# Optimization experiments

Hardware: AMD Instinct MI355X
Metric: run time of the kernel (lower is better)

Reference implementation:

```python
import jax, jax.numpy as jnp
import numpy as np

BATCH = 4
N_MELS, T_LEN, PATCH = 128, 512, 16
D_MODEL, D_INNER, D_STATE, DT_RANK, D_CONV = 512, 1024, 16, 32, 4
DEPTH, N_CLASSES = 4, 10


def _silu(x):
    return x * jax.nn.sigmoid(x)


def _ln(x, w, b):
    m = x.mean(-1, keepdims=True)
    v = ((x - m) ** 2).mean(-1, keepdims=True)
    return (x - m) * jax.lax.rsqrt(v + 1e-5) * w + b


def _causal_conv(x, w, b):
    # x: (B, L, D); w: (D, K) depthwise causal conv (mamba conv1d)
    K, L = w.shape[-1], x.shape[1]
    xp = jnp.pad(x, ((0, 0), (K - 1, 0), (0, 0)))
    y = sum(xp[:, k:k + L, :] * w[:, k] for k in range(K))
    return y + b


def _ssm(xc, conv_w, conv_b, xproj_w, dtproj_w, dtproj_b, A_log, Dp):
    # One directional selective scan (mamba S6).
    u = _silu(_causal_conv(xc, conv_w, conv_b))              # (B,L,Di)
    xdbl = jnp.einsum('bld,ed->ble', u, xproj_w)             # (B,L,dt_rank+2S)
    dtr, Bm, Cm = jnp.split(xdbl, [DT_RANK, DT_RANK + D_STATE], axis=-1)
    dt = jax.nn.softplus(jnp.einsum('blr,dr->bld', dtr, dtproj_w) + dtproj_b)
    A = -jnp.exp(A_log)                                      # (Di,S)
    dA = jnp.exp(dt[..., None] * A)                          # (B,L,Di,S)
    dBu = (dt * u)[..., None] * Bm[:, :, None, :]            # (B,L,Di,S)

    def comb(e1, e2):
        a1, b1 = e1
        a2, b2 = e2
        return a1 * a2, a2 * b1 + b2

    _, h = jax.lax.associative_scan(comb, (dA, dBu), axis=1)  # parallel linear recurrence
    return jnp.einsum('blds,bls->bld', h, Cm) + u * Dp


def _forward(x, patch_w, patch_b, in_proj_w, conv_w_f, conv_b_f, conv_w_b, conv_b_b,
             xproj_w_f, xproj_w_b, dtproj_w_f, dtproj_b_f, dtproj_w_b, dtproj_b_b,
             A_log_f, A_log_b, D_f, D_b, out_proj_w, norm_w, norm_b,
             normf_w, normf_b, ln_w, ln_b, fc1_w, fc1_b, fc2_w, fc2_b):
    B = x.shape[0]
    # Patch embed: conv with kernel == stride -> reshape + einsum
    xp = x.reshape(B, 1, N_MELS // PATCH, PATCH, T_LEN // PATCH, PATCH)
    tok = jnp.einsum('bchpwq,dcpq->bhwd', xp, patch_w) + patch_b
    h = tok.reshape(B, -1, D_MODEL)                           # (B, 256, D)
    for i in range(DEPTH):
        xn = _ln(h, norm_w[i], norm_b[i])
        xz = jnp.einsum('bld,ed->ble', xn, in_proj_w[i])
        xc, z = jnp.split(xz, 2, axis=-1)
        y_f = _ssm(xc, conv_w_f[i], conv_b_f[i], xproj_w_f[i],
                   dtproj_w_f[i], dtproj_b_f[i], A_log_f[i], D_f[i])
        y_b = jnp.flip(_ssm(jnp.flip(xc, 1), conv_w_b[i], conv_b_b[i], xproj_w_b[i],
                            dtproj_w_b[i], dtproj_b_b[i], A_log_b[i], D_b[i]), 1)
        y = (y_f + y_b) * _silu(z)                            # bimamba v2: fwd + flipped bwd, gated
        h = h + jnp.einsum('bld,ed->ble', y, out_proj_w[i])
    h = _ln(h, normf_w, normf_b)
    feat = h.mean(axis=1)                                     # pooled features (B, D)
    c = _ln(feat, ln_w, ln_b)
    c = jnp.maximum(c @ fc1_w.T + fc1_b, 0.0)
    return c @ fc2_w.T + fc2_b


def setup_inputs() -> dict:
    ks = iter(jax.random.split(jax.random.key(0), 64))

    def rn(shape, s=0.02):
        return jax.random.normal(next(ks), shape, jnp.float32) * s

    inp = {}
    inp['x'] = jax.random.normal(next(ks), (BATCH, 1, N_MELS, T_LEN), jnp.float32)
    inp['patch_w'] = rn((D_MODEL, 1, PATCH, PATCH))
    inp['patch_b'] = jnp.zeros((D_MODEL,), jnp.float32)
    inp['in_proj_w'] = rn((DEPTH, 2 * D_INNER, D_MODEL))
    A_init = jnp.log(jnp.tile(jnp.arange(1, D_STATE + 1, dtype=jnp.float32), (DEPTH, D_INNER, 1)))
    for sfx in ('f', 'b'):
        inp[f'conv_w_{sfx}'] = rn((DEPTH, D_INNER, D_CONV), 0.2)
        inp[f'conv_b_{sfx}'] = jnp.zeros((DEPTH, D_INNER), jnp.float32)
        inp[f'xproj_w_{sfx}'] = rn((DEPTH, DT_RANK + 2 * D_STATE, D_INNER))
        inp[f'dtproj_w_{sfx}'] = rn((DEPTH, D_INNER, DT_RANK), 0.1)
        inp[f'dtproj_b_{sfx}'] = jnp.full((DEPTH, D_INNER), -4.6, jnp.float32)  # softplus -> dt ~ 0.01
        inp[f'A_log_{sfx}'] = A_init
        inp[f'D_{sfx}'] = jnp.ones((DEPTH, D_INNER), jnp.float32)
    inp['out_proj_w'] = rn((DEPTH, D_MODEL, D_INNER))
    inp['norm_w'] = jnp.ones((DEPTH, D_MODEL), jnp.float32)
    inp['norm_b'] = jnp.zeros((DEPTH, D_MODEL), jnp.float32)
    inp['normf_w'] = jnp.ones((D_MODEL,), jnp.float32)
    inp['normf_b'] = jnp.zeros((D_MODEL,), jnp.float32)
    inp['ln_w'] = jnp.ones((D_MODEL,), jnp.float32)
    inp['ln_b'] = jnp.zeros((D_MODEL,), jnp.float32)
    inp['fc1_w'] = rn((512, D_MODEL))
    inp['fc1_b'] = jnp.zeros((512,), jnp.float32)
    inp['fc2_w'] = rn((N_CLASSES, 512))
    inp['fc2_b'] = jnp.zeros((N_CLASSES,), jnp.float32)
    return inp


def reference(x, patch_w, patch_b, in_proj_w, conv_w_f, conv_b_f, conv_w_b, conv_b_b,
              xproj_w_f, xproj_w_b, dtproj_w_f, dtproj_b_f, dtproj_w_b, dtproj_b_b,
              A_log_f, A_log_b, D_f, D_b, out_proj_w, norm_w, norm_b,
              normf_w, normf_b, ln_w, ln_b, fc1_w, fc1_b, fc2_w, fc2_b):
    return _forward(x, patch_w, patch_b, in_proj_w, conv_w_f, conv_b_f, conv_w_b, conv_b_b,
                    xproj_w_f, xproj_w_b, dtproj_w_f, dtproj_b_f, dtproj_w_b, dtproj_b_b,
                    A_log_f, A_log_b, D_f, D_b, out_proj_w, norm_w, norm_b,
                    normf_w, normf_b, ln_w, ln_b, fc1_w, fc1_b, fc2_w, fc2_b)
```

## Files before the change

kernel.cpp:

```cpp
#include <hip/hip_runtime.h>


#define BB 4
#define LL 256
#define DM 512
#define DI 1024
#define LDST 40

typedef unsigned short u16;
typedef unsigned int u32;
typedef __attribute__((ext_vector_type(8))) short s8v;
typedef __attribute__((ext_vector_type(4))) float f4v;

__device__ __forceinline__ float silu_f(float x){ return x/(1.f+__expf(-x)); }
__device__ __forceinline__ float b2f(u16 u){
  union { u32 i; float f; } v; v.i = ((u32)u) << 16; return v.f;
}
__device__ __forceinline__ void b2x2(u32 w, float& lo, float& hi){
  union { u32 i; float f; } a, b;
  a.i = w << 16; b.i = w & 0xffff0000u;
  lo = a.f; hi = b.f;
}
__device__ __forceinline__ u16 f2bf(float f){
  union { float f; u32 u; } v; v.f = f;
  u32 r = (v.u + 0x7fffu + ((v.u >> 16) & 1u)) >> 16;
  return (u16)r;
}

__device__ __forceinline__ float row_sum16(float p){
  union { float f; int i; } v, r;
  v.f = p;
  r.i = __builtin_amdgcn_update_dpp(0, v.i, 0x111, 0xF, 0xF, true); v.f += r.f;
  r.i = __builtin_amdgcn_update_dpp(0, v.i, 0x112, 0xF, 0xF, true); v.f += r.f;
  r.i = __builtin_amdgcn_update_dpp(0, v.i, 0x114, 0xF, 0xF, true); v.f += r.f;
  r.i = __builtin_amdgcn_update_dpp(0, v.i, 0x118, 0xF, 0xF, true); v.f += r.f;
  return v.f;
}

__device__ __forceinline__ void block_reduce2(float& a, float& b, float* sc, int nw){
  int lane = threadIdx.x & 63, wid = threadIdx.x >> 6;
#pragma unroll
  for (int o = 32; o > 0; o >>= 1){
    a += __shfl_down(a, o, 64);
    b += __shfl_down(b, o, 64);
  }
  if (lane == 0){ sc[wid*2] = a; sc[wid*2+1] = b; }
  __syncthreads();
  float ta = 0.f, tb = 0.f;
  for (int i = 0; i < nw; ++i){ ta += sc[i*2]; tb += sc[i*2+1]; }
  a = ta; b = tb;
}

__global__ __launch_bounds__(256) void convert_w(const float* __restrict__ inW,
    const float* __restrict__ outW, const float* __restrict__ xwF,
    const float* __restrict__ xwB, const float* __restrict__ dtwF,
    const float* __restrict__ dtwB, u16* __restrict__ inHi, u16* __restrict__ inLo,
    u16* __restrict__ outHi, u16* __restrict__ outLo, u16* __restrict__ xwHi,
    u16* __restrict__ xwLo, u16* __restrict__ dtwHi, u16* __restrict__ dtwLo){
  int idx = blockIdx.x*256 + threadIdx.x;
  const float4* src; ushort4* dh; ushort4* dl;
  if (idx < 262144){
    src = (const float4*)inW + idx;
    dh = (ushort4*)inHi + idx; dl = (ushort4*)inLo + idx;
  } else if (idx < 393216){
    int j = idx - 262144;
    src = (const float4*)outW + j;
    dh = (ushort4*)outHi + j; dl = (ushort4*)outLo + j;
  } else if (idx < 409600){
    int j = idx - 393216;
    src = (const float4*)xwF + j;
    dh = (ushort4*)xwHi + j; dl = (ushort4*)xwLo + j;
  } else if (idx < 425984){
    int j = idx - 409600;
    src = (const float4*)xwB + j;
    dh = (ushort4*)(xwHi + 65536) + j; dl = (ushort4*)(xwLo + 65536) + j;
  } else if (idx < 434176){
    int j = idx - 425984;
    src = (const float4*)dtwF + j;
    dh = (ushort4*)dtwHi + j; dl = (ushort4*)dtwLo + j;
  } else {
    int j = idx - 434176;
    src = (const float4*)dtwB + j;
    dh = (ushort4*)(dtwHi + 32768) + j; dl = (ushort4*)(dtwLo + 32768) + j;
  }
  float4 v = *src;
  ushort4 h, l;
  h.x = f2bf(v.x); l.x = f2bf(v.x - b2f(h.x));
  h.y = f2bf(v.y); l.y = f2bf(v.y - b2f(h.y));
  h.z = f2bf(v.z); l.z = f2bf(v.z - b2f(h.z));
  h.w = f2bf(v.w); l.w = f2bf(v.w - b2f(h.w));
  *dh = h; *dl = l;
}

__global__ __launch_bounds__(256) void patch_embed(const float* __restrict__ x,
    const float* __restrict__ pw, const float* __restrict__ pb, float* __restrict__ h){
  __shared__ float xs[8*256];
  int blk = blockIdx.x;
  int b = blk >> 6, ph = (blk >> 3) & 7, pg = (blk >> 1) & 3, dh = blk & 1;
  int t = threadIdx.x;
  for (int idx = t; idx < 2048; idx += 256){
    int j = idx >> 8, pix = idx & 255, p = pix >> 4, q = pix & 15;
    xs[idx] = x[(size_t)(b*128 + ph*16 + p)*512 + pg*128 + j*16 + q];
  }
  __syncthreads();
  int d = dh*256 + t;
  float acc[8] = {};
  const float* wr = pw + (size_t)d*256;
  for (int i = 0; i < 256; i += 8){
    float4 w0 = *(const float4*)(wr + i);
    float4 w1 = *(const float4*)(wr + i + 4);
    float wf[8] = {w0.x,w0.y,w0.z,w0.w,w1.x,w1.y,w1.z,w1.w};
#pragma unroll
    for (int j = 0; j < 8; ++j){
#pragma unroll
      for (int jj = 0; jj < 8; ++jj)
        acc[j] = fmaf(xs[j*256 + i + jj], wf[jj], acc[j]);
    }
  }
  float bias = pb[d];
#pragma unroll
  for (int j = 0; j < 8; ++j)
    h[(size_t)(b*256 + ph*32 + pg*8 + j)*512 + d] = acc[j] + bias;
}

__global__ __launch_bounds__(256) void prep_ln(const float* __restrict__ x,
    const float* __restrict__ w, const float* __restrict__ bias, int wOff,
    u16* __restrict__ hiO, u16* __restrict__ loO){
  __shared__ float sc[8];
  int row = blockIdx.x, t = threadIdx.x;
  const float* xr = x + (size_t)row*DM;
  float v0 = xr[t], v1 = xr[t + 256];
  float s = v0 + v1, ss = v0*v0 + v1*v1;
  block_reduce2(s, ss, sc, 4);
  float mean = s * (1.f/512.f);
  float var = ss * (1.f/512.f) - mean*mean;
  float inv = rsqrtf(var + 1e-5f);
  float o0 = (v0 - mean)*inv*w[wOff + t]       + bias[wOff + t];
  float o1 = (v1 - mean)*inv*w[wOff + t + 256] + bias[wOff + t + 256];
  u16 h0 = f2bf(o0), h1 = f2bf(o1);
  hiO[(size_t)row*DM + t]       = h0;
  hiO[(size_t)row*DM + t + 256] = h1;
  loO[(size_t)row*DM + t]       = f2bf(o0 - b2f(h0));
  loO[(size_t)row*DM + t + 256] = f2bf(o1 - b2f(h1));
}

__global__ __launch_bounds__(256) void prep_gate(const float* __restrict__ ybuf,
    const float* __restrict__ xz, u16* __restrict__ gHi, u16* __restrict__ gLo){
  int row = blockIdx.x, t = threadIdx.x;
  int c = t*4;
  float4 yf = *(const float4*)(ybuf + (size_t)row*DI + c);
  float4 yb = *(const float4*)(ybuf + 1048576 + (size_t)row*DI + c);
  float4 zv = *(const float4*)(xz + (size_t)row*2048 + 1024 + c);
  float g0 = (yf.x + yb.x)*silu_f(zv.x);
  float g1 = (yf.y + yb.y)*silu_f(zv.y);
  float g2 = (yf.z + yb.z)*silu_f(zv.z);
  float g3 = (yf.w + yb.w)*silu_f(zv.w);
  ushort4 h, l;
  h.x = f2bf(g0); l.x = f2bf(g0 - b2f(h.x));
  h.y = f2bf(g1); l.y = f2bf(g1 - b2f(h.y));
  h.z = f2bf(g2); l.z = f2bf(g2 - b2f(h.z));
  h.w = f2bf(g3); l.w = f2bf(g3 - b2f(h.w));
  *(ushort4*)(gHi + (size_t)row*DI + c) = h;
  *(ushort4*)(gLo + (size_t)row*DI + c) = l;
}

__global__ __launch_bounds__(256) void gemm_bf16(const u16* __restrict__ Ahi_g,
    const u16* __restrict__ Alo_g, int As, const u16* __restrict__ Bhi_g,
    const u16* __restrict__ Blo_g, int Bs, float* __restrict__ C, int Cs,
    int K, int addFlag){
  __shared__ __align__(16) u16 Ah[64*LDST], Al[64*LDST], Bh[64*LDST], Bl[64*LDST];
  int bm = blockIdx.y*64, bn = blockIdx.x*64;
  int t = threadIdx.x;
  int sr = t >> 2, sc8 = (t & 3)*8;
  int lane = t & 63, wv = t >> 6, ml = lane & 15, quad = lane >> 4;
  int mq = wv >> 1, nq = wv & 1;
  f4v acc[2][2] = {};
  for (int k0 = 0; k0 < K; k0 += 32){
    *(uint4*)&Ah[sr*LDST + sc8] = *(const uint4*)(Ahi_g + (size_t)(bm + sr)*As + k0 + sc8);
    *(uint4*)&Al[sr*LDST + sc8] = *(const uint4*)(Alo_g + (size_t)(bm + sr)*As + k0 + sc8);
    *(uint4*)&Bh[sr*LDST + sc8] = *(const uint4*)(Bhi_g + (size_t)(bn + sr)*Bs + k0 + sc8);
    *(uint4*)&Bl[sr*LDST + sc8] = *(const uint4*)(Blo_g + (size_t)(bn + sr)*Bs + k0 + sc8);
    __syncthreads();
    s8v ah[2], al2[2], bh2[2], bl2[2];
#pragma unroll
    for (int mt = 0; mt < 2; ++mt){
      int row = mq*32 + mt*16 + ml;
      ah[mt]  = *(s8v*)&Ah[row*LDST + quad*8];
      al2[mt] = *(s8v*)&Al[row*LDST + quad*8];
    }
#pragma unroll
    for (int nt = 0; nt < 2; ++nt){
      int col = nq*32 + nt*16 + ml;
      bh2[nt] = *(s8v*)&Bh[col*LDST + quad*8];
      bl2[nt] = *(s8v*)&Bl[col*LDST + quad*8];
    }
#pragma unroll
    for (int mt = 0; mt < 2; ++mt)
#pragma unroll
      for (int nt = 0; nt < 2; ++nt){
        acc[mt][nt] = __builtin_amdgcn_mfma_f32_16x16x32_bf16(ah[mt],  bh2[nt], acc[mt][nt], 0, 0, 0);
        acc[mt][nt] = __builtin_amdgcn_mfma_f32_16x16x32_bf16(al2[mt], bh2[nt], acc[mt][nt], 0, 0, 0);
        acc[mt][nt] = __builtin_amdgcn_mfma_f32_16x16x32_bf16(ah[mt],  bl2[nt], acc[mt][nt], 0, 0, 0);
      }
    __syncthreads();
  }
#pragma unroll
  for (int mt = 0; mt < 2; ++mt)
#pragma unroll
    for (int nt = 0; nt < 2; ++nt)
#pragma unroll
      for (int r = 0; r < 4; ++r){
        float* cp = C + (size_t)(bm + mq*32 + mt*16 + quad*4 + r)*Cs +
                    bn + nq*32 + nt*16 + ml;
        if (addFlag) *cp += acc[mt][nt][r];
        else         *cp  = acc[mt][nt][r];
      }
}

__global__ __launch_bounds__(256) void conv_silu_split(const float* __restrict__ xz,
    const float* __restrict__ cwF, const float* __restrict__ cbF,
    const float* __restrict__ cwB, const float* __restrict__ cbB,
    int cwOff, int cbOff, u16* __restrict__ uHi, u16* __restrict__ uLo){
  int blk = blockIdx.x;
  int dir = blk >> 8, rem = blk & 255, b = rem >> 6, lg = rem & 63;
  int l0 = lg*4;
  const float* cw = dir ? cwB : cwF;
  const float* cb = dir ? cbB : cbF;
  int t = threadIdx.x;
  int rbase = (dir*BB + b)*LL;
  for (int dd = 0; dd < 4; ++dd){
    int d = t + dd*256;
    float4 w4 = *(const float4*)(cw + cwOff + d*4);
    float wf[4] = {w4.x, w4.y, w4.z, w4.w};
    float bias = cb[cbOff + d];
#pragma unroll
    for (int r = 0; r < 4; ++r){
      int l = l0 + r;
      float acc = bias;
#pragma unroll
      for (int k = 0; k < 4; ++k){
        int li = l + k - 3;
        if (li >= 0){
          int sl = dir ? (LL-1-li) : li;
          acc = fmaf(xz[(size_t)(b*LL + sl)*2048 + d], wf[k], acc);
        }
      }
      float uval = silu_f(acc);
      u16 h = f2bf(uval);
      uHi[(size_t)(rbase + l)*DI + d] = h;
      uLo[(size_t)(rbase + l)*DI + d] = f2bf(uval - b2f(h));
    }
  }
}

__global__ __launch_bounds__(256) void gemm_xproj(const u16* __restrict__ uHi,
    const u16* __restrict__ uLo, const u16* __restrict__ xwHi,
    const u16* __restrict__ xwLo, float* __restrict__ xdbl,
    u16* __restrict__ dtrHi, u16* __restrict__ dtrLo){
  __shared__ __align__(16) u16 Ah[64*LDST], Al[64*LDST], Bh[64*LDST], Bl[64*LDST];
  int bm = blockIdx.y*64;
  int dir = bm >> 10;
  const u16* BhG = xwHi + dir*65536;
  const u16* BlG = xwLo + dir*65536;
  int t = threadIdx.x;
  int sr = t >> 2, sc8 = (t & 3)*8;
  int lane = t & 63, wv = t >> 6, ml = lane & 15, quad = lane >> 4;
  int mq = wv >> 1, nq = wv & 1;
  f4v acc[2][2] = {};
  for (int k0 = 0; k0 < 1024; k0 += 32){
    *(uint4*)&Ah[sr*LDST + sc8] = *(const uint4*)(uHi + (size_t)(bm + sr)*1024 + k0 + sc8);
    *(uint4*)&Al[sr*LDST + sc8] = *(const uint4*)(uLo + (size_t)(bm + sr)*1024 + k0 + sc8);
    *(uint4*)&Bh[sr*LDST + sc8] = *(const uint4*)(BhG + (size_t)sr*1024 + k0 + sc8);
    *(uint4*)&Bl[sr*LDST + sc8] = *(const uint4*)(BlG + (size_t)sr*1024 + k0 + sc8);
    __syncthreads();
    s8v ah[2], al2[2], bh2[2], bl2[2];
#pragma unroll
    for (int mt = 0; mt < 2; ++mt){
      int row = mq*32 + mt*16 + ml;
      ah[mt]  = *(s8v*)&Ah[row*LDST + quad*8];
      al2[mt] = *(s8v*)&Al[row*LDST + quad*8];
    }
#pragma unroll
    for (int nt = 0; nt < 2; ++nt){
      int col = nq*32 + nt*16 + ml;
      bh2[nt] = *(s8v*)&Bh[col*LDST + quad*8];
      bl2[nt] = *(s8v*)&Bl[col*LDST + quad*8];
    }
#pragma unroll
    for (int mt = 0; mt < 2; ++mt)
#pragma unroll
      for (int nt = 0; nt < 2; ++nt){
        acc[mt][nt] = __builtin_amdgcn_mfma_f32_16x16x32_bf16(ah[mt],  bh2[nt], acc[mt][nt], 0, 0, 0);
        acc[mt][nt] = __builtin_amdgcn_mfma_f32_16x16x32_bf16(al2[mt], bh2[nt], acc[mt][nt], 0, 0, 0);
        acc[mt][nt] = __builtin_amdgcn_mfma_f32_16x16x32_bf16(ah[mt],  bl2[nt], acc[mt][nt], 0, 0, 0);
      }
    __syncthreads();
  }
#pragma unroll
  for (int mt = 0; mt < 2; ++mt)
#pragma unroll
    for (int nt = 0; nt < 2; ++nt){
      int col = nq*32 + nt*16 + ml;
#pragma unroll
      for (int r = 0; r < 4; ++r){
        int row = bm + mq*32 + mt*16 + quad*4 + r;
        float v = acc[mt][nt][r];
        xdbl[(size_t)row*64 + col] = v;
        if (nq == 0){
          u16 h = f2bf(v);
          dtrHi[(size_t)row*32 + col] = h;
          dtrLo[(size_t)row*32 + col] = f2bf(v - b2f(h));
        }
      }
    }
}

__global__ __launch_bounds__(256) void gemm_dt(const u16* __restrict__ dtrHi,
    const u16* __restrict__ dtrLo, const u16* __restrict__ dtwHi,
    const u16* __restrict__ dtwLo, const float* __restrict__ dtbF,
    const float* __restrict__ dtbB, int bOff, float* __restrict__ dtOut){
  __shared__ __align__(16) u16 Ah[64*LDST], Al[64*LDST], Bh[64*LDST], Bl[64*LDST];
  int bm = blockIdx.y*64, bn = blockIdx.x*64;
  int dir = bm >> 10;
  const u16* BhG = dtwHi + dir*32768;
  const u16* BlG = dtwLo + dir*32768;
  const float* dtb = dir ? dtbB : dtbF;
  int t = threadIdx.x;
  int sr = t >> 2, sc8 = (t & 3)*8;
  int lane = t & 63, wv = t >> 6, ml = lane & 15, quad = lane >> 4;
  int mq = wv >> 1, nq = wv & 1;
  *(uint4*)&Ah[sr*LDST + sc8] = *(const uint4*)(dtrHi + (size_t)(bm + sr)*32 + sc8);
  *(uint4*)&Al[sr*LDST + sc8] = *(const uint4*)(dtrLo + (size_t)(bm + sr)*32 + sc8);
  *(uint4*)&Bh[sr*LDST + sc8] = *(const uint4*)(BhG + (size_t)(bn + sr)*32 + sc8);
  *(uint4*)&Bl[sr*LDST + sc8] = *(const uint4*)(BlG + (size_t)(bn + sr)*32 + sc8);
  __syncthreads();
  f4v acc[2][2] = {};
  s8v ah[2], al2[2], bh2[2], bl2[2];
#pragma unroll
  for (int mt = 0; mt < 2; ++mt){
    int row = mq*32 + mt*16 + ml;
    ah[mt]  = *(s8v*)&Ah[row*LDST + quad*8];
    al2[mt] = *(s8v*)&Al[row*LDST + quad*8];
  }
#pragma unroll
  for (int nt = 0; nt < 2; ++nt){
    int col = nq*32 + nt*16 + ml;
    bh2[nt] = *(s8v*)&Bh[col*LDST + quad*8];
    bl2[nt] = *(s8v*)&Bl[col*LDST + quad*8];
  }
#pragma unroll
  for (int mt = 0; mt < 2; ++mt)
#pragma unroll
    for (int nt = 0; nt < 2; ++nt){
      acc[mt][nt] = __builtin_amdgcn_mfma_f32_16x16x32_bf16(ah[mt],  bh2[nt], acc[mt][nt], 0, 0, 0);
      acc[mt][nt] = __builtin_amdgcn_mfma_f32_16x16x32_bf16(al2[mt], bh2[nt], acc[mt][nt], 0, 0, 0);
      acc[mt][nt] = __builtin_amdgcn_mfma_f32_16x16x32_bf16(ah[mt],  bl2[nt], acc[mt][nt], 0, 0, 0);
    }
#pragma unroll
  for (int mt = 0; mt < 2; ++mt)
#pragma unroll
    for (int nt = 0; nt < 2; ++nt){
      int col = bn + nq*32 + nt*16 + ml;
      float bias = dtb[bOff + col];
#pragma unroll
      for (int r = 0; r < 4; ++r){
        int row = bm + mq*32 + mt*16 + quad*4 + r;
        float sv = acc[mt][nt][r] + bias;
        dtOut[(size_t)row*1024 + col] = (sv > 15.f) ? sv : log1pf(__expf(sv));
      }
    }
}

__global__ __launch_bounds__(256) void scan_coal(const float* __restrict__ dt,
    const u16* __restrict__ uHi, const u16* __restrict__ uLo,
    const float* __restrict__ xd,
    const float* __restrict__ AlogF, const float* __restrict__ AlogB,
    const float* __restrict__ DF, const float* __restrict__ DB,
    int aOff, int dOff, float* __restrict__ y){
  __shared__ __align__(16) float dtuT[16][516];
  __shared__ __align__(16) float BCT[16][516];
  __shared__ __align__(16) float ytile[128][16];
  int blk = blockIdx.x;
  int dir = blk >> 8, b = (blk >> 6) & 3, dg = blk & 63;
  int t = threadIdx.x;
  int rbase = (dir*BB + b)*LL;
  const float* Alog = dir ? AlogB : AlogF;
  const float* Dpt  = dir ? DB : DF;
  {
    int q = t & 3, lb = t >> 2;
    for (int pass = 0; pass < 4; ++pass){
      int l = pass*64 + lb;
      size_t base = (size_t)(rbase + l)*DI + dg*16 + q*4;
      float4 dv = *(const float4*)(dt + base);
      uint2 uh = *(const uint2*)(uHi + base);
      uint2 ul = *(const uint2*)(uLo + base);
      float h0,h1,h2,h3,l0f,l1f,l2f,l3f;
      b2x2(uh.x, h0, h1); b2x2(uh.y, h2, h3);
      b2x2(ul.x, l0f, l1f); b2x2(ul.y, l2f, l3f);
      float2 p0 = {dv.x, h0 + l0f}, p1 = {dv.y, h1 + l1f};
      float2 p2 = {dv.z, h2 + l2f}, p3 = {dv.w, h3 + l3f};
      *(float2*)&dtuT[q*4+0][l*2] = p0;
      *(float2*)&dtuT[q*4+1][l*2] = p1;
      *(float2*)&dtuT[q*4+2][l*2] = p2;
      *(float2*)&dtuT[q*4+3][l*2] = p3;
    }
  }
  {
    int h8 = t & 7, lb = t >> 3;
    for (int pass = 0; pass < 8; ++pass){
      int l = pass*32 + lb;
      float4 v = *(const float4*)(xd + (size_t)(rbase + l)*64 + 32 + h8*4);
      if (h8 < 4){
        int s0 = h8*4;
        BCT[s0+0][l*2] = v.x; BCT[s0+1][l*2] = v.y;
        BCT[s0+2][l*2] = v.z; BCT[s0+3][l*2] = v.w;
      } else {
        int s0 = (h8-4)*4;
        BCT[s0+0][l*2+1] = v.x; BCT[s0+1][l*2+1] = v.y;
        BCT[s0+2][l*2+1] = v.z; BCT[s0+3][l*2+1] = v.w;
      }
    }
  }
  int s = t & 15, dl = t >> 4;
  float Av = -__expf(Alog[aOff + dg*256 + t]);
  float Dp = Dpt[dOff + dg*16 + dl];
  __syncthreads();
  float h = 0.f;
  for (int half = 0; half < 2; ++half){
    for (int l0 = half*128; l0 < half*128 + 128; l0 += 4){
      float4 du01 = *(const float4*)&dtuT[dl][l0*2];
      float4 du23 = *(const float4*)&dtuT[dl][l0*2 + 4];
      float4 bc01 = *(const float4*)&BCT[s][l0*2];
      float4 bc23 = *(const float4*)&BCT[s][l0*2 + 4];
      float dtv[4] = {du01.x, du01.z, du23.x, du23.z};
      float uv[4]  = {du01.y, du01.w, du23.y, du23.w};
      float Bv[4]  = {bc01.x, bc01.z, bc23.x, bc23.z};
      float Cv[4]  = {bc01.y, bc01.w, bc23.y, bc23.w};
#pragma unroll
      for (int i = 0; i < 4; ++i){
        float a = __expf(dtv[i] * Av);
        h = fmaf(a, h, dtv[i]*uv[i]*Bv[i]);
        float p = h * Cv[i];
        float sum = row_sum16(p);
        if (s == 15){
          int lr = (l0 + i) & 127;
          ytile[lr][dl] = fmaf(uv[i], Dp, sum);
        }
      }
    }
    __syncthreads();
    {
      int d4 = t & 3, lh = t >> 2;
      for (int pass = 0; pass < 2; ++pass){
        int lr = pass*64 + lh;
        int l = half*128 + lr;
        int lo = dir ? (255 - l) : l;
        float4 vv = *(const float4*)&ytile[lr][d4*4];
        *(float4*)(y + (size_t)(rbase + lo)*DI + dg*16 + d4*4) = vv;
      }
    }
    __syncthreads();
  }
}

__global__ __launch_bounds__(256) void ln_kernel(const float* __restrict__ x,
    const float* __restrict__ w, const float* __restrict__ bias,
    float* __restrict__ y){
  __shared__ float sc[8];
  int row = blockIdx.x, t = threadIdx.x;
  const float* xr = x + (size_t)row*DM;
  float v0 = xr[t], v1 = xr[t + 256];
  float s = v0 + v1, ss = v0*v0 + v1*v1;
  block_reduce2(s, ss, sc, 4);
  float mean = s * (1.f/512.f);
  float var = ss * (1.f/512.f) - mean*mean;
  float inv = rsqrtf(var + 1e-5f);
  float* yr = y + (size_t)row*DM;
  yr[t]       = (v0 - mean)*inv*w[t]       + bias[t];
  yr[t + 256] = (v1 - mean)*inv*w[t + 256] + bias[t + 256];
}

__global__ __launch_bounds__(256) void pool_kernel(const float* __restrict__ hn,
    float* __restrict__ feat){
  __shared__ float part[4][64];
  int b = blockIdx.x >> 3, dg = blockIdx.x & 7;
  int t = threadIdx.x, dl = t & 63, lq = t >> 6;
  const float* p = hn + (size_t)(b*256 + lq*64)*512 + dg*64 + dl;
  float s = 0.f;
#pragma unroll 4
  for (int i = 0; i < 64; ++i) s += p[(size_t)i*512];
  part[lq][dl] = s;
  __syncthreads();
  if (t < 64)
    feat[b*512 + dg*64 + t] =
        (part[0][t] + part[1][t] + part[2][t] + part[3][t]) * (1.f/256.f);
}

__global__ __launch_bounds__(512) void head_kernel(const float* __restrict__ feat,
    const float* __restrict__ lnw, const float* __restrict__ lnb,
    const float* __restrict__ fc1w, const float* __restrict__ fc1b,
    const float* __restrict__ fc2w, const float* __restrict__ fc2b,
    float* __restrict__ out){
  __shared__ float sc[16];
  __shared__ float cbuf[512];
  __shared__ float rbuf[512];
  int b = blockIdx.x, t = threadIdx.x;
  float v = feat[b*512 + t];
  float s = v, ss = v*v;
  block_reduce2(s, ss, sc, 8);
  float mean = s * (1.f/512.f);
  float var = ss * (1.f/512.f) - mean*mean;
  float inv = rsqrtf(var + 1e-5f);
  cbuf[t] = (v - mean)*inv*lnw[t] + lnb[t];
  __syncthreads();
  float a = fc1b[t];
  const float* w1 = fc1w + (size_t)t*512;
  for (int i = 0; i < 512; i += 8){
    float4 w0 = *(const float4*)(w1 + i);
    float4 w4 = *(const float4*)(w1 + i + 4);
    float wf[8] = {w0.x,w0.y,w0.z,w0.w,w4.x,w4.y,w4.z,w4.w};
#pragma unroll
    for (int j = 0; j < 8; ++j) a = fmaf(cbuf[i + j], wf[j], a);
  }
  rbuf[t] = fmaxf(a, 0.f);
  __syncthreads();
  if (t < 10){
    float a2 = fc2b[t];
    const float* w2 = fc2w + (size_t)t*512;
    for (int i = 0; i < 512; ++i) a2 = fmaf(rbuf[i], w2[i], a2);
    out[b*10 + t] = a2;
  }
}

extern "C" void kernel_launch(void* const* d_in, const int* in_sizes, int n_in,
                              void* d_out, int out_size, void* d_ws, size_t ws_size,
                              hipStream_t stream) {
  (void)in_sizes; (void)n_in; (void)out_size; (void)ws_size;
  const float* x          = (const float*)d_in[0];
  const float* patch_w    = (const float*)d_in[1];
  const float* patch_b    = (const float*)d_in[2];
  const float* in_proj_w  = (const float*)d_in[3];
  const float* conv_w_f   = (const float*)d_in[4];
  const float* conv_b_f   = (const float*)d_in[5];
  const float* xproj_w_f  = (const float*)d_in[6];
  const float* dtproj_w_f = (const float*)d_in[7];
  const float* dtproj_b_f = (const float*)d_in[8];
  const float* A_log_f    = (const float*)d_in[9];
  const float* D_f        = (const float*)d_in[10];
  const float* conv_w_b   = (const float*)d_in[11];
  const float* conv_b_b   = (const float*)d_in[12];
  const float* xproj_w_b  = (const float*)d_in[13];
  const float* dtproj_w_b = (const float*)d_in[14];
  const float* dtproj_b_b = (const float*)d_in[15];
  const float* A_log_b    = (const float*)d_in[16];
  const float* D_b        = (const float*)d_in[17];
  const float* out_proj_w = (const float*)d_in[18];
  const float* norm_w     = (const float*)d_in[19];
  const float* norm_b     = (const float*)d_in[20];
  const float* normf_w    = (const float*)d_in[21];
  const float* normf_b    = (const float*)d_in[22];
  const float* ln_w       = (const float*)d_in[23];
  const float* ln_b       = (const float*)d_in[24];
  const float* fc1_w      = (const float*)d_in[25];
  const float* fc1_b      = (const float*)d_in[26];
  const float* fc2_w      = (const float*)d_in[27];
  const float* fc2_b      = (const float*)d_in[28];

  float* ws   = (float*)d_ws;
  float* hbuf = ws;
  float* xz   = ws + 524288;
  u16*   uHi  = (u16*)(ws + 2621440);
  u16*   uLo  = (u16*)(ws + 2621440 + 1048576);
  float* xdbl = ws + 4718592;
  float* dtbuf= ws + 4849664;
  float* ybuf = ws + 6946816;
  u16*   xwHi = (u16*)(ws + 6946816);
  u16*   xwLo = (u16*)(ws + 7012352);
  u16*   dtwHi= (u16*)(ws + 7077888);
  u16*   dtwLo= (u16*)(ws + 7110656);
  u16*   dtrHi= (u16*)(ws + 7143424);
  u16*   dtrLo= (u16*)(ws + 7176192);
  float* hn   = ws + 9043968;
  u16*   inHi = (u16*)(ws + 9568256);
  u16*   inLo = (u16*)(ws + 10092544);
  u16*   outHi= (u16*)(ws + 10616832);
  u16*   outLo= (u16*)(ws + 10878976);
  float* feat = ws + 11141120;
  u16*   xnHi = (u16*)hn;
  u16*   xnLo = (u16*)(ws + 9043968 + 262144);
  u16*   gHi  = (u16*)(ws + 2621440);
  u16*   gLo  = (u16*)(ws + 2621440 + 524288);

  patch_embed<<<256, 256, 0, stream>>>(x, patch_w, patch_b, hbuf);
  for (int i = 0; i < 4; ++i){
    convert_w<<<1728, 256, 0, stream>>>(
        in_proj_w + (size_t)i*1048576, out_proj_w + (size_t)i*524288,
        xproj_w_f + (size_t)i*65536, xproj_w_b + (size_t)i*65536,
        dtproj_w_f + (size_t)i*32768, dtproj_w_b + (size_t)i*32768,
        inHi, inLo, outHi, outLo, xwHi, xwLo, dtwHi, dtwLo);
    prep_ln<<<1024, 256, 0, stream>>>(hbuf, norm_w, norm_b, i*512, xnHi, xnLo);
    gemm_bf16<<<dim3(32, 16), 256, 0, stream>>>(
        xnHi, xnLo, 512, inHi, inLo, 512, xz, 2048, 512, 0);
    conv_silu_split<<<512, 256, 0, stream>>>(
        xz, conv_w_f, conv_b_f, conv_w_b, conv_b_b, i*4096, i*1024, uHi, uLo);
    gemm_xproj<<<dim3(1, 32), 256, 0, stream>>>(
        uHi, uLo, xwHi, xwLo, xdbl, dtrHi, dtrLo);
    gemm_dt<<<dim3(16, 32), 256, 0, stream>>>(
        dtrHi, dtrLo, dtwHi, dtwLo, dtproj_b_f, dtproj_b_b, i*1024, dtbuf);
    scan_coal<<<512, 256, 0, stream>>>(
        dtbuf, uHi, uLo, xdbl, A_log_f, A_log_b, D_f, D_b, i*16384, i*1024, ybuf);
    prep_gate<<<1024, 256, 0, stream>>>(ybuf, xz, gHi, gLo);
    gemm_bf16<<<dim3(8, 16), 256, 0, stream>>>(
        gHi, gLo, 1024, outHi, outLo, 1024, hbuf, 512, 1024, 1);
  }
  ln_kernel<<<1024, 256, 0, stream>>>(hbuf, normf_w, normf_b, hn);
  pool_kernel<<<32, 256, 0, stream>>>(hn, feat);
  head_kernel<<<4, 512, 0, stream>>>(feat, ln_w, ln_b, fc1_w, fc1_b, fc2_w, fc2_b,
                                     (float*)d_out);
}
```

Baseline: 691.0 us.

## Fuse dt projection into x-proj GEMM and gate into bidirectional scan

The dt_rank projection GEMM now runs inside the x-projection kernel, which keeps the dtr tile in shared memory and loops over all 1024 output columns. The scan kernel now handles both directions in one block and applies the silu(z) gate with the hi/lo bf16 split directly, so the separate prep_gate kernel and the ybuf round trip are gone. This removes two launches and several global-memory passes. In exchange, the dt GEMM now runs on only 32 blocks instead of 512, and the scan grid is halved with the two directions serialized, which cuts parallelism on a large GPU.

```diff
diff --git a/kernel.cpp b/kernel.cpp
--- a/kernel.cpp
+++ b/kernel.cpp
@@ -144,26 +144,6 @@
   loO[(size_t)row*DM + t + 256] = f2bf(o1 - b2f(h1));
 }
 
-__global__ __launch_bounds__(256) void prep_gate(const float* __restrict__ ybuf,
-    const float* __restrict__ xz, u16* __restrict__ gHi, u16* __restrict__ gLo){
-  int row = blockIdx.x, t = threadIdx.x;
-  int c = t*4;
-  float4 yf = *(const float4*)(ybuf + (size_t)row*DI + c);
-  float4 yb = *(const float4*)(ybuf + 1048576 + (size_t)row*DI + c);
-  float4 zv = *(const float4*)(xz + (size_t)row*2048 + 1024 + c);
-  float g0 = (yf.x + yb.x)*silu_f(zv.x);
-  float g1 = (yf.y + yb.y)*silu_f(zv.y);
-  float g2 = (yf.z + yb.z)*silu_f(zv.z);
-  float g3 = (yf.w + yb.w)*silu_f(zv.w);
-  ushort4 h, l;
-  h.x = f2bf(g0); l.x = f2bf(g0 - b2f(h.x));
-  h.y = f2bf(g1); l.y = f2bf(g1 - b2f(h.y));
-  h.z = f2bf(g2); l.z = f2bf(g2 - b2f(h.z));
-  h.w = f2bf(g3); l.w = f2bf(g3 - b2f(h.w));
-  *(ushort4*)(gHi + (size_t)row*DI + c) = h;
-  *(ushort4*)(gLo + (size_t)row*DI + c) = l;
-}
-
 __global__ __launch_bounds__(256) void gemm_bf16(const u16* __restrict__ Ahi_g,
     const u16* __restrict__ Alo_g, int As, const u16* __restrict__ Bhi_g,
     const u16* __restrict__ Blo_g, int Bs, float* __restrict__ C, int Cs,
@@ -253,11 +233,14 @@
   }
 }
 
-__global__ __launch_bounds__(256) void gemm_xproj(const u16* __restrict__ uHi,
+__global__ __launch_bounds__(256) void gemm_xproj_dt(const u16* __restrict__ uHi,
     const u16* __restrict__ uLo, const u16* __restrict__ xwHi,
-    const u16* __restrict__ xwLo, float* __restrict__ xdbl,
-    u16* __restrict__ dtrHi, u16* __restrict__ dtrLo){
+    const u16* __restrict__ xwLo, const u16* __restrict__ dtwHi,
+    const u16* __restrict__ dtwLo, const float* __restrict__ dtbF,
+    const float* __restrict__ dtbB, int bOff,
+    float* __restrict__ xdbl, float* __restrict__ dtOut){
   __shared__ __align__(16) u16 Ah[64*LDST], Al[64*LDST], Bh[64*LDST], Bl[64*LDST];
+  __shared__ __align__(16) u16 DtrH[64*LDST], DtrL[64*LDST];
   int bm = blockIdx.y*64;
   int dir = bm >> 10;
   const u16* BhG = xwHi + dir*65536;
@@ -303,163 +286,185 @@
       int col = nq*32 + nt*16 + ml;
 #pragma unroll
       for (int r = 0; r < 4; ++r){
-        int row = bm + mq*32 + mt*16 + quad*4 + r;
+        int lrow = mq*32 + mt*16 + quad*4 + r;
         float v = acc[mt][nt][r];
-        xdbl[(size_t)row*64 + col] = v;
+        xdbl[(size_t)(bm + lrow)*64 + col] = v;
         if (nq == 0){
           u16 h = f2bf(v);
-          dtrHi[(size_t)row*32 + col] = h;
-          dtrLo[(size_t)row*32 + col] = f2bf(v - b2f(h));
+          DtrH[lrow*LDST + col] = h;
+          DtrL[lrow*LDST + col] = f2bf(v - b2f(h));
         }
       }
     }
-}
-
-__global__ __launch_bounds__(256) void gemm_dt(const u16* __restrict__ dtrHi,
-    const u16* __restrict__ dtrLo, const u16* __restrict__ dtwHi,
-    const u16* __restrict__ dtwLo, const float* __restrict__ dtbF,
-    const float* __restrict__ dtbB, int bOff, float* __restrict__ dtOut){
-  __shared__ __align__(16) u16 Ah[64*LDST], Al[64*LDST], Bh[64*LDST], Bl[64*LDST];
-  int bm = blockIdx.y*64, bn = blockIdx.x*64;
-  int dir = bm >> 10;
-  const u16* BhG = dtwHi + dir*32768;
-  const u16* BlG = dtwLo + dir*32768;
+  __syncthreads();
+  const u16* DhG = dtwHi + dir*32768;
+  const u16* DlG = dtwLo + dir*32768;
   const float* dtb = dir ? dtbB : dtbF;
-  int t = threadIdx.x;
-  int sr = t >> 2, sc8 = (t & 3)*8;
-  int lane = t & 63, wv = t >> 6, ml = lane & 15, quad = lane >> 4;
-  int mq = wv >> 1, nq = wv & 1;
-  *(uint4*)&Ah[sr*LDST + sc8] = *(const uint4*)(dtrHi + (size_t)(bm + sr)*32 + sc8);
-  *(uint4*)&Al[sr*LDST + sc8] = *(const uint4*)(dtrLo + (size_t)(bm + sr)*32 + sc8);
-  *(uint4*)&Bh[sr*LDST + sc8] = *(const uint4*)(BhG + (size_t)(bn + sr)*32 + sc8);
-  *(uint4*)&Bl[sr*LDST + sc8] = *(const uint4*)(BlG + (size_t)(bn + sr)*32 + sc8);
-  __syncthreads();
-  f4v acc[2][2] = {};
-  s8v ah[2], al2[2], bh2[2], bl2[2];
-#pragma unroll
-  for (int mt = 0; mt < 2; ++mt){
-    int row = mq*32 + mt*16 + ml;
-    ah[mt]  = *(s8v*)&Ah[row*LDST + quad*8];
-    al2[mt] = *(s8v*)&Al[row*LDST + quad*8];
-  }
-#pragma unroll
-  for (int nt = 0; nt < 2; ++nt){
-    int col = nq*32 + nt*16 + ml;
-    bh2[nt] = *(s8v*)&Bh[col*LDST + quad*8];
-    bl2[nt] = *(s8v*)&Bl[col*LDST + quad*8];
-  }
-#pragma unroll
-  for (int mt = 0; mt < 2; ++mt)
+  for (int nt0 = 0; nt0 < 1024; nt0 += 64){
+    *(uint4*)&Bh[sr*LDST + sc8] = *(const uint4*)(DhG + (size_t)(nt0 + sr)*32 + sc8);
+    *(uint4*)&Bl[sr*LDST + sc8] = *(const uint4*)(DlG + (size_t)(nt0 + sr)*32 + sc8);
+    __syncthreads();
+    f4v acc2[2][2] = {};
+    s8v ah[2], al2[2], bh2[2], bl2[2];
+#pragma unroll
+    for (int mt = 0; mt < 2; ++mt){
+      int row = mq*32 + mt*16 + ml;
+      ah[mt]  = *(s8v*)&DtrH[row*LDST + quad*8];
+      al2[mt] = *(s8v*)&DtrL[row*LDST + quad*8];
+    }
 #pragma unroll
     for (int nt = 0; nt < 2; ++nt){
-      acc[mt][nt] = __builtin_amdgcn_mfma_f32_16x16x32_bf16(ah[mt],  bh2[nt], acc[mt][nt], 0, 0, 0);
-      acc[mt][nt] = __builtin_amdgcn_mfma_f32_16x16x32_bf16(al2[mt], bh2[nt], acc[mt][nt], 0, 0, 0);
-      acc[mt][nt] = __builtin_amdgcn_mfma_f32_16x16x32_bf16(ah[mt],  bl2[nt], acc[mt][nt], 0, 0, 0);
-    }
-#pragma unroll
-  for (int mt = 0; mt < 2; ++mt)
-#pragma unroll
-    for (int nt = 0; nt < 2; ++nt){
-      int col = bn + nq*32 + nt*16 + ml;
-      float bias = dtb[bOff + col];
-#pragma unroll
-      for (int r = 0; r < 4; ++r){
-        int row = bm + mq*32 + mt*16 + quad*4 + r;
-        float sv = acc[mt][nt][r] + bias;
-        dtOut[(size_t)row*1024 + col] = (sv > 15.f) ? sv : log1pf(__expf(sv));
-      }
-    }
-}
-
-__global__ __launch_bounds__(256) void scan_coal(const float* __restrict__ dt,
+      int col = nq*32 + nt*16 + ml;
+      bh2[nt] = *(s8v*)&Bh[col*LDST + quad*8];
+      bl2[nt] = *(s8v*)&Bl[col*LDST + quad*8];
+    }
+#pragma unroll
+    for (int mt = 0; mt < 2; ++mt)
+#pragma unroll
+      for (int nt = 0; nt < 2; ++nt){
+        acc2[mt][nt] = __builtin_amdgcn_mfma_f32_16x16x32_bf16(ah[mt],  bh2[nt], acc2[mt][nt], 0, 0, 0);
+        acc2[mt][nt] = __builtin_amdgcn_mfma_f32_16x16x32_bf16(al2[mt], bh2[nt], acc2[mt][nt], 0, 0, 0);
+        acc2[mt][nt] = __builtin_amdgcn_mfma_f32_16x16x32_bf16(ah[mt],  bl2[nt], acc2[mt][nt], 0, 0, 0);
+      }
+#pragma unroll
+    for (int mt = 0; mt < 2; ++mt)
+#pragma unroll
+      for (int nt = 0; nt < 2; ++nt){
+        int gcol = nt0 + nq*32 + nt*16 + ml;
+        float bias = dtb[bOff + gcol];
+#pragma unroll
+        for (int r = 0; r < 4; ++r){
+          int grow = bm + mq*32 + mt*16 + quad*4 + r;
+          float sv = acc2[mt][nt][r] + bias;
+          dtOut[(size_t)grow*1024 + gcol] = (sv > 15.f) ? sv : log1pf(__expf(sv));
+        }
+      }
+    __syncthreads();
+  }
+}
+
+__global__ __launch_bounds__(256) void scan_gate(const float* __restrict__ dt,
     const u16* __restrict__ uHi, const u16* __restrict__ uLo,
-    const float* __restrict__ xd,
+    const float* __restrict__ xd, const float* __restrict__ xz,
     const float* __restrict__ AlogF, const float* __restrict__ AlogB,
     const float* __restrict__ DF, const float* __restrict__ DB,
-    int aOff, int dOff, float* __restrict__ y){
+    int aOff, int dOff, u16* __restrict__ gHi, u16* __restrict__ gLo){
   __shared__ __align__(16) float dtuT[16][516];
   __shared__ __align__(16) float BCT[16][516];
-  __shared__ __align__(16) float ytile[128][16];
+  __shared__ __align__(16) float yfull[256][20];
+  __shared__ __align__(16) float ybt[128][20];
   int blk = blockIdx.x;
-  int dir = blk >> 8, b = (blk >> 6) & 3, dg = blk & 63;
+  int b = blk >> 6, dg = blk & 63;
   int t = threadIdx.x;
-  int rbase = (dir*BB + b)*LL;
-  const float* Alog = dir ? AlogB : AlogF;
-  const float* Dpt  = dir ? DB : DF;
-  {
-    int q = t & 3, lb = t >> 2;
-    for (int pass = 0; pass < 4; ++pass){
-      int l = pass*64 + lb;
-      size_t base = (size_t)(rbase + l)*DI + dg*16 + q*4;
-      float4 dv = *(const float4*)(dt + base);
-      uint2 uh = *(const uint2*)(uHi + base);
-      uint2 ul = *(const uint2*)(uLo + base);
-      float h0,h1,h2,h3,l0f,l1f,l2f,l3f;
-      b2x2(uh.x, h0, h1); b2x2(uh.y, h2, h3);
-      b2x2(ul.x, l0f, l1f); b2x2(ul.y, l2f, l3f);
-      float2 p0 = {dv.x, h0 + l0f}, p1 = {dv.y, h1 + l1f};
-      float2 p2 = {dv.z, h2 + l2f}, p3 = {dv.w, h3 + l3f};
-      *(float2*)&dtuT[q*4+0][l*2] = p0;
-      *(float2*)&dtuT[q*4+1][l*2] = p1;
-      *(float2*)&dtuT[q*4+2][l*2] = p2;
-      *(float2*)&dtuT[q*4+3][l*2] = p3;
-    }
-  }
-  {
-    int h8 = t & 7, lb = t >> 3;
-    for (int pass = 0; pass < 8; ++pass){
-      int l = pass*32 + lb;
-      float4 v = *(const float4*)(xd + (size_t)(rbase + l)*64 + 32 + h8*4);
-      if (h8 < 4){
-        int s0 = h8*4;
-        BCT[s0+0][l*2] = v.x; BCT[s0+1][l*2] = v.y;
-        BCT[s0+2][l*2] = v.z; BCT[s0+3][l*2] = v.w;
-      } else {
-        int s0 = (h8-4)*4;
-        BCT[s0+0][l*2+1] = v.x; BCT[s0+1][l*2+1] = v.y;
-        BCT[s0+2][l*2+1] = v.z; BCT[s0+3][l*2+1] = v.w;
-      }
-    }
-  }
   int s = t & 15, dl = t >> 4;
-  float Av = -__expf(Alog[aOff + dg*256 + t]);
-  float Dp = Dpt[dOff + dg*16 + dl];
-  __syncthreads();
-  float h = 0.f;
-  for (int half = 0; half < 2; ++half){
-    for (int l0 = half*128; l0 < half*128 + 128; l0 += 4){
-      float4 du01 = *(const float4*)&dtuT[dl][l0*2];
-      float4 du23 = *(const float4*)&dtuT[dl][l0*2 + 4];
-      float4 bc01 = *(const float4*)&BCT[s][l0*2];
-      float4 bc23 = *(const float4*)&BCT[s][l0*2 + 4];
-      float dtv[4] = {du01.x, du01.z, du23.x, du23.z};
-      float uv[4]  = {du01.y, du01.w, du23.y, du23.w};
-      float Bv[4]  = {bc01.x, bc01.z, bc23.x, bc23.z};
-      float Cv[4]  = {bc01.y, bc01.w, bc23.y, bc23.w};
-#pragma unroll
-      for (int i = 0; i < 4; ++i){
-        float a = __expf(dtv[i] * Av);
-        h = fmaf(a, h, dtv[i]*uv[i]*Bv[i]);
-        float p = h * Cv[i];
-        float sum = row_sum16(p);
-        if (s == 15){
-          int lr = (l0 + i) & 127;
-          ytile[lr][dl] = fmaf(uv[i], Dp, sum);
+  float AvF = -__expf(AlogF[aOff + dg*256 + t]);
+  float AvB = -__expf(AlogB[aOff + dg*256 + t]);
+  float DpF = DF[dOff + dg*16 + dl];
+  float DpB = DB[dOff + dg*16 + dl];
+#pragma unroll
+  for (int dirp = 0; dirp < 2; ++dirp){
+    int rbase = (dirp*BB + b)*LL;
+    {
+      int q = t & 3, lb = t >> 2;
+      for (int pass = 0; pass < 4; ++pass){
+        int l = pass*64 + lb;
+        size_t base = (size_t)(rbase + l)*DI + dg*16 + q*4;
+        float4 dv = *(const float4*)(dt + base);
+        uint2 uh = *(const uint2*)(uHi + base);
+        uint2 ul = *(const uint2*)(uLo + base);
+        float h0,h1,h2,h3,l0f,l1f,l2f,l3f;
+        b2x2(uh.x, h0, h1); b2x2(uh.y, h2, h3);
+        b2x2(ul.x, l0f, l1f); b2x2(ul.y, l2f, l3f);
+        float2 p0 = {dv.x, h0 + l0f}, p1 = {dv.y, h1 + l1f};
+        float2 p2 = {dv.z, h2 + l2f}, p3 = {dv.w, h3 + l3f};
+        *(float2*)&dtuT[q*4+0][l*2] = p0;
+        *(float2*)&dtuT[q*4+1][l*2] = p1;
+        *(float2*)&dtuT[q*4+2][l*2] = p2;
+        *(float2*)&dtuT[q*4+3][l*2] = p3;
+      }
+      int h8 = t & 7, lb8 = t >> 3;
+      for (int pass = 0; pass < 8; ++pass){
+        int l = pass*32 + lb8;
+        float4 v = *(const float4*)(xd + (size_t)(rbase + l)*64 + 32 + h8*4);
+        if (h8 < 4){
+          int s0 = h8*4;
+          BCT[s0+0][l*2] = v.x; BCT[s0+1][l*2] = v.y;
+          BCT[s0+2][l*2] = v.z; BCT[s0+3][l*2] = v.w;
+        } else {
+          int s0 = (h8-4)*4;
+          BCT[s0+0][l*2+1] = v.x; BCT[s0+1][l*2+1] = v.y;
+          BCT[s0+2][l*2+1] = v.z; BCT[s0+3][l*2+1] = v.w;
         }
       }
     }
     __syncthreads();
-    {
-      int d4 = t & 3, lh = t >> 2;
-      for (int pass = 0; pass < 2; ++pass){
-        int lr = pass*64 + lh;
-        int l = half*128 + lr;
-        int lo = dir ? (255 - l) : l;
-        float4 vv = *(const float4*)&ytile[lr][d4*4];
-        *(float4*)(y + (size_t)(rbase + lo)*DI + dg*16 + d4*4) = vv;
-      }
-    }
-    __syncthreads();
+    float Av = dirp ? AvB : AvF;
+    float Dp = dirp ? DpB : DpF;
+    float h = 0.f;
+    if (dirp == 0){
+      for (int l0 = 0; l0 < 256; l0 += 4){
+        float4 du01 = *(const float4*)&dtuT[dl][l0*2];
+        float4 du23 = *(const float4*)&dtuT[dl][l0*2 + 4];
+        float4 bc01 = *(const float4*)&BCT[s][l0*2];
+        float4 bc23 = *(const float4*)&BCT[s][l0*2 + 4];
+        float dtv[4] = {du01.x, du01.z, du23.x, du23.z};
+        float uv[4]  = {du01.y, du01.w, du23.y, du23.w};
+        float Bv[4]  = {bc01.x, bc01.z, bc23.x, bc23.z};
+        float Cv[4]  = {bc01.y, bc01.w, bc23.y, bc23.w};
+#pragma unroll
+        for (int i = 0; i < 4; ++i){
+          float a = __expf(dtv[i] * Av);
+          h = fmaf(a, h, dtv[i]*uv[i]*Bv[i]);
+          float sum = row_sum16(h * Cv[i]);
+          if (s == 15) yfull[l0 + i][dl] = fmaf(uv[i], Dp, sum);
+        }
+      }
+      __syncthreads();
+    } else {
+      for (int half = 0; half < 2; ++half){
+        for (int l0 = half*128; l0 < half*128 + 128; l0 += 4){
+          float4 du01 = *(const float4*)&dtuT[dl][l0*2];
+          float4 du23 = *(const float4*)&dtuT[dl][l0*2 + 4];
+          float4 bc01 = *(const float4*)&BCT[s][l0*2];
+          float4 bc23 = *(const float4*)&BCT[s][l0*2 + 4];
+          float dtv[4] = {du01.x, du01.z, du23.x, du23.z};
+          float uv[4]  = {du01.y, du01.w, du23.y, du23.w};
+          float Bv[4]  = {bc01.x, bc01.z, bc23.x, bc23.z};
+          float Cv[4]  = {bc01.y, bc01.w, bc23.y, bc23.w};
+#pragma unroll
+          for (int i = 0; i < 4; ++i){
+            float a = __expf(dtv[i] * Av);
+            h = fmaf(a, h, dtv[i]*uv[i]*Bv[i]);
+            float sum = row_sum16(h * Cv[i]);
+            if (s == 15) ybt[(l0 + i) & 127][dl] = fmaf(uv[i], Dp, sum);
+          }
+        }
+        __syncthreads();
+        {
+          int d4 = t & 3, lh = t >> 2;
+          for (int pass = 0; pass < 2; ++pass){
+            int lr = pass*64 + lh;
+            int lo = 255 - (half*128 + lr);
+            float4 yf4 = *(float4*)&yfull[lo][d4*4];
+            float4 yb4 = *(float4*)&ybt[lr][d4*4];
+            float4 z4 = *(const float4*)(xz + (size_t)(b*256 + lo)*2048 + 1024 + dg*16 + d4*4);
+            float g0 = (yf4.x + yb4.x)*silu_f(z4.x);
+            float g1 = (yf4.y + yb4.y)*silu_f(z4.y);
+            float g2 = (yf4.z + yb4.z)*silu_f(z4.z);
+            float g3 = (yf4.w + yb4.w)*silu_f(z4.w);
+            ushort4 hh, ll;
+            hh.x = f2bf(g0); ll.x = f2bf(g0 - b2f(hh.x));
+            hh.y = f2bf(g1); ll.y = f2bf(g1 - b2f(hh.y));
+            hh.z = f2bf(g2); ll.z = f2bf(g2 - b2f(hh.z));
+            hh.w = f2bf(g3); ll.w = f2bf(g3 - b2f(hh.w));
+            size_t go = (size_t)(b*256 + lo)*1024 + dg*16 + d4*4;
+            *(ushort4*)(gHi + go) = hh;
+            *(ushort4*)(gLo + go) = ll;
+          }
+        }
+        __syncthreads();
+      }
+    }
   }
 }
 
@@ -570,16 +575,15 @@
   float* hbuf = ws;
   float* xz   = ws + 524288;
   u16*   uHi  = (u16*)(ws + 2621440);
-  u16*   uLo  = (u16*)(ws + 2621440 + 1048576);
+  u16*   uLo  = (u16*)(ws + 3670016);
   float* xdbl = ws + 4718592;
   float* dtbuf= ws + 4849664;
-  float* ybuf = ws + 6946816;
   u16*   xwHi = (u16*)(ws + 6946816);
   u16*   xwLo = (u16*)(ws + 7012352);
   u16*   dtwHi= (u16*)(ws + 7077888);
   u16*   dtwLo= (u16*)(ws + 7110656);
-  u16*   dtrHi= (u16*)(ws + 7143424);
-  u16*   dtrLo= (u16*)(ws + 7176192);
+  u16*   gHi  = (u16*)(ws + 7143424);
+  u16*   gLo  = (u16*)(ws + 7667712);
   float* hn   = ws + 9043968;
   u16*   inHi = (u16*)(ws + 9568256);
   u16*   inLo = (u16*)(ws + 10092544);
@@ -587,9 +591,7 @@
   u16*   outLo= (u16*)(ws + 10878976);
   float* feat = ws + 11141120;
   u16*   xnHi = (u16*)hn;
-  u16*   xnLo = (u16*)(ws + 9043968 + 262144);
-  u16*   gHi  = (u16*)(ws + 2621440);
-  u16*   gLo  = (u16*)(ws + 2621440 + 524288);
+  u16*   xnLo = (u16*)(ws + 9306112);
 
   patch_embed<<<256, 256, 0, stream>>>(x, patch_w, patch_b, hbuf);
   for (int i = 0; i < 4; ++i){
@@ -603,13 +605,12 @@
         xnHi, xnLo, 512, inHi, inLo, 512, xz, 2048, 512, 0);
     conv_silu_split<<<512, 256, 0, stream>>>(
         xz, conv_w_f, conv_b_f, conv_w_b, conv_b_b, i*4096, i*1024, uHi, uLo);
-    gemm_xproj<<<dim3(1, 32), 256, 0, stream>>>(
-        uHi, uLo, xwHi, xwLo, xdbl, dtrHi, dtrLo);
-    gemm_dt<<<dim3(16, 32), 256, 0, stream>>>(
-        dtrHi, dtrLo, dtwHi, dtwLo, dtproj_b_f, dtproj_b_b, i*1024, dtbuf);
-    scan_coal<<<512, 256, 0, stream>>>(
-        dtbuf, uHi, uLo, xdbl, A_log_f, A_log_b, D_f, D_b, i*16384, i*1024, ybuf);
-    prep_gate<<<1024, 256, 0, stream>>>(ybuf, xz, gHi, gLo);
+    gemm_xproj_dt<<<dim3(1, 32), 256, 0, stream>>>(
+        uHi, uLo, xwHi, xwLo, dtwHi, dtwLo, dtproj_b_f, dtproj_b_b, i*1024,
+        xdbl, dtbuf);
+    scan_gate<<<256, 256, 0, stream>>>(
+        dtbuf, uHi, uLo, xdbl, xz, A_log_f, A_log_b, D_f, D_b,
+        i*16384, i*1024, gHi, gLo);
     gemm_bf16<<<dim3(8, 16), 256, 0, stream>>>(
         gHi, gLo, 1024, outHi, outLo, 1024, hbuf, 512, 1024, 1);
   }
```

After: 1.078 ms. 1.56x slower.
